# Optimization experiments

Hardware: AMD Instinct MI355X
Metric: run time of the kernel (lower is better)

The kernel has to match this reference:

```python
import jax, jax.numpy as jnp
import numpy as np

D_MODEL = 1024
N_HEADS = 16
HEAD_DIM = D_MODEL // N_HEADS
ROPE_BASE = 10000.0
NEG_INF = -1.0e9


def rotate_half(x):
    # interleaved pairs: (-x2_i, x1_i) re-flattened to last dim
    x1 = x[..., ::2]
    x2 = x[..., 1::2]
    return jnp.stack((-x2, x1), axis=-1).reshape(x.shape)


def rope_sin_cos(seq_len, head_dim, dtype):
    inv_freq = 1.0 / (ROPE_BASE ** (jnp.arange(0, head_dim, 2, dtype=jnp.float32) / head_dim))
    t = jnp.arange(seq_len, dtype=jnp.float32)
    freqs = jnp.einsum('i,j->ij', t, inv_freq)          # [T, hd/2]
    emb = jnp.concatenate((freqs, freqs), axis=-1)       # [T, hd]
    return jnp.sin(emb).astype(dtype), jnp.cos(emb).astype(dtype)


def apply_rope(x, sin, cos):
    # x: [B, H, T, hd]; sin/cos: [T, hd]
    return x * cos[None, None] + rotate_half(x) * sin[None, None]


def setup_inputs() -> dict:
    key = jax.random.key(0)
    ks = jax.random.split(key, 9)
    B, T, D = 2, 2048, D_MODEL
    q = jax.random.normal(ks[0], (B, T, D), dtype=jnp.float32)
    k = jax.random.normal(ks[1], (B, T, D), dtype=jnp.float32)
    v = jax.random.normal(ks[2], (B, T, D), dtype=jnp.float32)
    # causal additive mask, broadcastable over [B, H, Tq, Tk]
    causal = jnp.triu(jnp.full((T, T), NEG_INF, dtype=jnp.float32), k=1)
    attn_mask = causal[None, None]
    key_padding_mask = jax.random.uniform(ks[3], (B, T)) < 0.05
    scale = 1.0 / np.sqrt(D)
    Wq = jax.random.normal(ks[4], (D, D), dtype=jnp.float32) * scale
    Wk = jax.random.normal(ks[5], (D, D), dtype=jnp.float32) * scale
    Wv = jax.random.normal(ks[6], (D, D), dtype=jnp.float32) * scale
    Wo = jax.random.normal(ks[7], (D, D), dtype=jnp.float32) * scale
    return {"q": q, "k": k, "v": v, "attn_mask": attn_mask,
            "key_padding_mask": key_padding_mask,
            "Wq": Wq, "Wk": Wk, "Wv": Wv, "Wo": Wo}


def reference(q, k, v, attn_mask, key_padding_mask, Wq, Wk, Wv, Wo):
    B, Tq, _ = q.shape
    Tk = k.shape[1]
    H, hd = N_HEADS, HEAD_DIM
    # projections (nn.Linear: x @ W.T), split heads -> [B, H, T, hd]
    qh = (q @ Wq.T).reshape(B, Tq, H, hd).transpose(0, 2, 1, 3)
    kh = (k @ Wk.T).reshape(B, Tk, H, hd).transpose(0, 2, 1, 3)
    vh = (v @ Wv.T).reshape(B, Tk, H, hd).transpose(0, 2, 1, 3)
    sin_q, cos_q = rope_sin_cos(Tq, hd, q.dtype)
    sin_k, cos_k = rope_sin_cos(Tk, hd, k.dtype)
    qh = apply_rope(qh, sin_q, cos_q)
    kh = apply_rope(kh, sin_k, cos_k)
    scores = jnp.einsum('bhqd,bhkd->bhqk', qh, kh) / np.sqrt(hd)
    scores = scores + attn_mask
    scores = jnp.where(key_padding_mask[:, None, None, :], NEG_INF, scores)
    attn = jax.nn.softmax(scores, axis=-1)
    out = jnp.einsum('bhqk,bhkd->bhqd', attn, vh)
    out = out.transpose(0, 2, 1, 3).reshape(B, Tq, H * hd)
    return out @ Wo.T
```

## Files before the change

kernel.cpp:

```cpp
#include <hip/hip_runtime.h>
#include <stdint.h>

typedef __bf16 bf16x8 __attribute__((ext_vector_type(8)));
typedef float f32x4 __attribute__((ext_vector_type(4)));
typedef float f32x16 __attribute__((ext_vector_type(16)));

#define NEG_BIG2 (-1.442695040e9f)
#define SC_LOG2  (0.180336880f)

__device__ __forceinline__ unsigned short f2b(float f) {
  union { float f; unsigned int u; } c; c.f = f;
  unsigned int u = c.u;
  u += 0x7FFFu + ((u >> 16) & 1u);
  return (unsigned short)(u >> 16);
}
__device__ __forceinline__ float b2f(unsigned short h) {
  union { unsigned int u; float f; } c; c.u = ((unsigned int)h) << 16;
  return c.f;
}
__device__ __forceinline__ unsigned int pk2(float a, float b) {
  __bf16 x = (__bf16)a, y = (__bf16)b;
  unsigned short xu, yu;
  __builtin_memcpy(&xu, &x, 2);
  __builtin_memcpy(&yu, &y, 2);
  return (unsigned)xu | ((unsigned)yu << 16);
}
__device__ __forceinline__ float ex2(float x) {
  float r; asm("v_exp_f32 %0, %1" : "=v"(r) : "v"(x)); return r;
}

typedef const __attribute__((address_space(1))) unsigned int ga_u32;
typedef __attribute__((address_space(3))) unsigned int ls_u32;
__device__ __forceinline__ void gld16(const void* g, void* l) {
  __builtin_amdgcn_global_load_lds((ga_u32*)g, (ls_u32*)l, 16, 0, 0);
}

__device__ __forceinline__ void swap_pair(unsigned a, unsigned b, int hi,
                                          unsigned& lo_out, unsigned& hi_out) {
#if __has_builtin(__builtin_amdgcn_permlane32_swap)
  auto r = __builtin_amdgcn_permlane32_swap(a, b, false, false);
  lo_out = r[0]; hi_out = r[1];
#else
  unsigned pa = __shfl_xor(a, 32), pb = __shfl_xor(b, 32);
  lo_out = hi ? pb : a;
  hi_out = hi ? b : pa;
#endif
}

__global__ void rope_table_k(float* __restrict__ sin_t, float* __restrict__ cos_t) {
  int i = blockIdx.x * blockDim.x + threadIdx.x;
  int t = i >> 6, d = i & 63, f = d & 31;
  double inv = exp(-((double)(2 * f) / 64.0) * log(10000.0));
  double ang = (double)t * inv;
  sin_t[i] = (float)sin(ang);
  cos_t[i] = (float)cos(ang);
}

__global__ void detect_mask_k(const unsigned int* __restrict__ kpm, int* __restrict__ flag) {
  unsigned int v = 0;
  for (int i = threadIdx.x; i < 1024; i += 256) v |= kpm[i];
  if (v & ~1u) atomicOr(flag, 1);
}

__global__ void mask_pack_k(const void* __restrict__ kpm, const int* __restrict__ mflag,
                            unsigned long long* __restrict__ pmask) {
  const int w = threadIdx.x >> 6, lane = threadIdx.x & 63;
  const int bytes = *mflag;
  for (int i = w; i < 64; i += 4) {
    int b = i >> 5, kb = i & 31;
    int idx = b * 2048 + kb * 64 + lane;
    int pad = bytes ? (int)((const unsigned char*)kpm)[idx] : ((const int*)kpm)[idx];
    unsigned long long pm = __ballot(pad != 0);
    if (lane == 0) pmask[i] = pm;
  }
}

__global__ void convw_k(const float* __restrict__ Wq, const float* __restrict__ Wk,
                        const float* __restrict__ Wv, const float* __restrict__ Wo,
                        unsigned short* __restrict__ Wb) {
  size_t g = (size_t)blockIdx.x * 256 + threadIdx.x;
  size_t i8 = g * 8;
  int t = (int)(i8 >> 20);
  const float* src = (t == 0 ? Wq : t == 1 ? Wk : t == 2 ? Wv : Wo) + (i8 & 1048575);
  float4 a = *(const float4*)src, c = *(const float4*)(src + 4);
  uint4 o = { pk2(a.x, a.y), pk2(a.z, a.w), pk2(c.x, c.y), pk2(c.z, c.w) };
  *(uint4*)&Wb[i8] = o;
}

__global__ void conv_in_k(const float* __restrict__ q, const float* __restrict__ k,
                          const float* __restrict__ v, unsigned short* __restrict__ qb,
                          unsigned short* __restrict__ kb, unsigned short* __restrict__ vb) {
  size_t g = (size_t)blockIdx.x * 256 + threadIdx.x;
  size_t i8 = g * 8;
  int t = (int)(i8 >> 22);
  size_t off = i8 & 4194303;
  const float* src = (t == 0 ? q : t == 1 ? k : v) + off;
  unsigned short* dst = (t == 0 ? qb : t == 1 ? kb : vb) + off;
  float4 a = *(const float4*)src, c = *(const float4*)(src + 4);
  uint4 o = { pk2(a.x, a.y), pk2(a.z, a.w), pk2(c.x, c.y), pk2(c.z, c.w) };
  *(uint4*)dst = o;
}

template<bool ABF>
__global__ __launch_bounds__(256) void qkv_k(const void* __restrict__ A0,
                                             const void* __restrict__ A1,
                                             const void* __restrict__ A2,
                                             const unsigned short* __restrict__ Wb,
                                             unsigned short* __restrict__ qh,
                                             unsigned short* __restrict__ kh,
                                             unsigned short* __restrict__ vt) {
  const int z = blockIdx.z;
  const void* Ap = (z == 0) ? A0 : (z == 1) ? A1 : A2;
  const unsigned short* Wp = Wb + (size_t)z * 1048576;
  unsigned short* outp = (z == 0) ? qh : (z == 1) ? kh : vt;

  __shared__ unsigned short As[128 * 32];
  __shared__ unsigned short Bs[128 * 32];
  const int M0 = blockIdx.x * 128, N0 = blockIdx.y * 128;
  const int tid = threadIdx.x, lane = tid & 63, w = tid >> 6;
  const int wr = w >> 1, wc = w & 1;
  const int lrow = lane & 15, lgrp = lane >> 4;

  const f32x4 Z4 = {0.f, 0.f, 0.f, 0.f};
  f32x4 acc[4][4];
#pragma unroll
  for (int i = 0; i < 4; ++i)
#pragma unroll
    for (int j = 0; j < 4; ++j) acc[i][j] = Z4;

  for (int kt = 0; kt < 1024; kt += 32) {
    __syncthreads();
    if (ABF) {
      const unsigned short* Ab = (const unsigned short*)Ap;
#pragma unroll
      for (int i = 0; i < 2; ++i) {
        const unsigned short* gA = Ab +
            (size_t)(M0 + i * 64 + w * 16 + (lane >> 2)) * 1024 + kt + (lane & 3) * 8;
        gld16(gA, &As[i * 2048 + w * 512]);
      }
    } else {
      const int row = tid >> 1, half = tid & 1;
      const float* ap = (const float*)Ap + (size_t)(M0 + row) * 1024 + kt + half * 16;
      float4 f0 = *(const float4*)ap, f1 = *(const float4*)(ap + 4);
      float4 f2 = *(const float4*)(ap + 8), f3 = *(const float4*)(ap + 12);
      uint4 u0 = { pk2(f0.x, f0.y), pk2(f0.z, f0.w), pk2(f1.x, f1.y), pk2(f1.z, f1.w) };
      uint4 u1 = { pk2(f2.x, f2.y), pk2(f2.z, f2.w), pk2(f3.x, f3.y), pk2(f3.z, f3.w) };
      *(uint4*)&As[row * 32 + half * 16] = u0;
      *(uint4*)&As[row * 32 + half * 16 + 8] = u1;
    }
#pragma unroll
    for (int i = 0; i < 2; ++i) {
      const unsigned short* gB = Wp +
          (size_t)(N0 + i * 64 + w * 16 + (lane >> 2)) * 1024 + kt + (lane & 3) * 8;
      gld16(gB, &Bs[i * 2048 + w * 512]);
    }
    __syncthreads();
    bf16x8 af[4], bfv[4];
#pragma unroll
    for (int m = 0; m < 4; ++m)
      af[m] = *(const bf16x8*)&As[(wr * 64 + m * 16 + lrow) * 32 + lgrp * 8];
#pragma unroll
    for (int n = 0; n < 4; ++n)
      bfv[n] = *(const bf16x8*)&Bs[(wc * 64 + n * 16 + lrow) * 32 + lgrp * 8];
    __builtin_amdgcn_s_setprio(1);
#pragma unroll
    for (int m = 0; m < 4; ++m)
#pragma unroll
      for (int n = 0; n < 4; ++n)
        acc[m][n] = __builtin_amdgcn_mfma_f32_16x16x32_bf16(af[m], bfv[n], acc[m][n], 0, 0, 0);
    __builtin_amdgcn_s_setprio(0);
  }

#pragma unroll
  for (int mi = 0; mi < 4; ++mi)
#pragma unroll
    for (int ni = 0; ni < 4; ++ni) {
      const int m = M0 + wr * 64 + mi * 16 + lgrp * 4;
      const int n = N0 + wc * 64 + ni * 16 + lrow;
      const int b = m >> 11, t = m & 2047;
      if (z < 2) {
        unsigned short* o = outp +
            ((size_t)(b * 16 + (n >> 6)) * 2048 + t) * 64 + (n & 63);
#pragma unroll
        for (int r = 0; r < 4; ++r) o[(size_t)r * 64] = f2b(acc[mi][ni][r]);
      } else {
        unsigned short* o = outp +
            ((size_t)(b * 16 + (n >> 6)) * 64 + (n & 63)) * 2048 + t;
        *(ushort4*)o = make_ushort4(f2b(acc[mi][ni][0]), f2b(acc[mi][ni][1]),
                                    f2b(acc[mi][ni][2]), f2b(acc[mi][ni][3]));
      }
    }
}

__global__ __launch_bounds__(256) void gemm_o_k(const unsigned short* __restrict__ Ab,
                                                const unsigned short* __restrict__ Wp,
                                                float* __restrict__ outp) {
  __shared__ unsigned short As[64 * 32];
  __shared__ unsigned short Bs[128 * 32];
  const int M0 = blockIdx.x * 64, N0 = blockIdx.y * 128;
  const int tid = threadIdx.x, lane = tid & 63, w = tid >> 6;
  const int wr = w >> 1, wc = w & 1;
  const int lrow = lane & 15, lgrp = lane >> 4;

  const f32x4 Z4 = {0.f, 0.f, 0.f, 0.f};
  f32x4 acc[2][4];
#pragma unroll
  for (int i = 0; i < 2; ++i)
#pragma unroll
    for (int j = 0; j < 4; ++j) acc[i][j] = Z4;

  for (int kt = 0; kt < 1024; kt += 32) {
    __syncthreads();
    {
      const unsigned short* gA = Ab +
          (size_t)(M0 + w * 16 + (lane >> 2)) * 1024 + kt + (lane & 3) * 8;
      gld16(gA, &As[w * 512]);
    }
#pragma unroll
    for (int i = 0; i < 2; ++i) {
      const unsigned short* gB = Wp +
          (size_t)(N0 + i * 64 + w * 16 + (lane >> 2)) * 1024 + kt + (lane & 3) * 8;
      gld16(gB, &Bs[i * 2048 + w * 512]);
    }
    __syncthreads();
    bf16x8 af[2], bfv[4];
#pragma unroll
    for (int m = 0; m < 2; ++m)
      af[m] = *(const bf16x8*)&As[(wr * 32 + m * 16 + lrow) * 32 + lgrp * 8];
#pragma unroll
    for (int n = 0; n < 4; ++n)
      bfv[n] = *(const bf16x8*)&Bs[(wc * 64 + n * 16 + lrow) * 32 + lgrp * 8];
    __builtin_amdgcn_s_setprio(1);
#pragma unroll
    for (int m = 0; m < 2; ++m)
#pragma unroll
      for (int n = 0; n < 4; ++n)
        acc[m][n] = __builtin_amdgcn_mfma_f32_16x16x32_bf16(af[m], bfv[n], acc[m][n], 0, 0, 0);
    __builtin_amdgcn_s_setprio(0);
  }

#pragma unroll
  for (int mi = 0; mi < 2; ++mi)
#pragma unroll
    for (int ni = 0; ni < 4; ++ni) {
      const int m = M0 + wr * 32 + mi * 16 + lgrp * 4;
      const int n = N0 + wc * 64 + ni * 16 + lrow;
      float* o = outp + (size_t)m * 1024 + n;
#pragma unroll
      for (int r = 0; r < 4; ++r) o[(size_t)r * 1024] = acc[mi][ni][r];
    }
}

__global__ void rope_apply_k(unsigned short* __restrict__ qh, unsigned short* __restrict__ kh,
                             const float* __restrict__ sin_t, const float* __restrict__ cos_t) {
  const size_t per = (size_t)2 * 16 * 2048 * 16;
  size_t gid = (size_t)blockIdx.x * blockDim.x + threadIdx.x;
  if (gid >= 2 * per) return;
  unsigned short* base = (gid < per) ? qh : kh;
  size_t g = (gid < per) ? gid : gid - per;
  const int t = (int)((g >> 4) & 2047);
  const int d0 = ((int)g & 15) * 4;
  ushort4 x = ((ushort4*)base)[g];
  const float4 s4 = *(const float4*)&sin_t[t * 64 + d0];
  const float4 c4 = *(const float4*)&cos_t[t * 64 + d0];
  float x0 = b2f(x.x), x1 = b2f(x.y), x2 = b2f(x.z), x3 = b2f(x.w);
  ushort4 o;
  o.x = f2b(x0 * c4.x - x1 * s4.x);
  o.y = f2b(x1 * c4.y + x0 * s4.y);
  o.z = f2b(x2 * c4.z - x3 * s4.z);
  o.w = f2b(x3 * c4.w + x2 * s4.w);
  ((ushort4*)base)[g] = o;
}

__global__ __launch_bounds__(256, 2) void attn_k(
    const unsigned short* __restrict__ qh, const unsigned short* __restrict__ kh,
    const unsigned short* __restrict__ vt, const unsigned long long* __restrict__ pmask,
    unsigned short* __restrict__ ao) {
  const int bid = blockIdx.x;
  const int x = bid & 7, g = bid >> 3;
  const int bh = x * 4 + (g & 3);
  const int tile = 15 - (g >> 2);
  const int b = bh >> 4, h = bh & 15;
  const int tid = threadIdx.x, lane = tid & 63, w = tid >> 6;
  const int ln31 = lane & 31, hi = lane >> 5;

  __shared__ char Kb[2][8192];
  __shared__ char Vb[2][8192];
  __shared__ int flagv;

  const size_t bh_off = (size_t)bh * 2048 * 64;
  const int qw = tile * 128 + w * 32;
  const int q_abs = qw + ln31;
  const int nkv_w = qw / 64 + 1;
  const int nkv_b = tile * 2 + 2;
  const int swz = (ln31 & 7) << 4;

  bf16x8 qf[4];
#pragma unroll
  for (int dc = 0; dc < 4; ++dc)
    qf[dc] = *(const bf16x8*)(qh + bh_off + (size_t)(qw + ln31) * 64 + dc * 16 + hi * 8);

  const f32x16 Z16 = {0.f,0.f,0.f,0.f,0.f,0.f,0.f,0.f,0.f,0.f,0.f,0.f,0.f,0.f,0.f,0.f};
  f32x16 O0 = Z16, O1 = Z16;
  float m_run = -INFINITY, l_run = 0.f;

  uint4 kr0, kr1, vr0, vr1;
  const int srow = tid >> 2, sseg = tid & 3;
  const int sbase = srow * 128 + sseg * 32;
  const int sswz = (srow & 7) << 4;

  auto stage_load = [&](int kbi) {
    const unsigned short* kp = kh + bh_off + (size_t)(kbi * 64 + srow) * 64 + sseg * 16;
    kr0 = *(const uint4*)kp; kr1 = *(const uint4*)(kp + 8);
    const unsigned short* vp = vt + bh_off + (size_t)srow * 2048 + kbi * 64 + sseg * 16;
    vr0 = *(const uint4*)vp; vr1 = *(const uint4*)(vp + 8);
  };
  auto stage_write = [&](int bu) {
    *(uint4*)(Kb[bu] + (sbase ^ sswz)) = kr0;
    *(uint4*)(Kb[bu] + ((sbase + 16) ^ sswz)) = kr1;
    *(uint4*)(Vb[bu] + (sbase ^ sswz)) = vr0;
    *(uint4*)(Vb[bu] + ((sbase + 16) ^ sswz)) = vr1;
  };

  auto compute = [&](int kb, int cur) {
    const unsigned long long pmh = pmask[b * 32 + kb] >> (hi * 4);
    f32x16 S0 = Z16, S1 = Z16;
    __builtin_amdgcn_s_setprio(1);
#pragma unroll
    for (int dc = 0; dc < 4; ++dc) {
      bf16x8 k0 = *(const bf16x8*)(Kb[cur] + ((ln31 * 128 + dc * 32 + hi * 16) ^ swz));
      bf16x8 k1 = *(const bf16x8*)(Kb[cur] + (((ln31 + 32) * 128 + dc * 32 + hi * 16) ^ swz));
      S0 = __builtin_amdgcn_mfma_f32_32x32x16_bf16(k0, qf[dc], S0, 0, 0, 0);
      S1 = __builtin_amdgcn_mfma_f32_32x32x16_bf16(k1, qf[dc], S1, 0, 0, 0);
    }
    __builtin_amdgcn_s_setprio(0);

    const bool diag = (kb * 64 + 63) > qw;
    if (diag) {
#pragma unroll
      for (int r = 0; r < 16; ++r) {
        const int kloc = (r & 3) + 8 * (r >> 2);
        float sv = S0[r] * SC_LOG2;
        sv = ((pmh >> kloc) & 1) ? NEG_BIG2
             : ((kb * 64 + kloc + 4 * hi > q_abs) ? sv + NEG_BIG2 : sv);
        S0[r] = sv;
        float sw = S1[r] * SC_LOG2;
        sw = ((pmh >> (kloc + 32)) & 1) ? NEG_BIG2
             : ((kb * 64 + 32 + kloc + 4 * hi > q_abs) ? sw + NEG_BIG2 : sw);
        S1[r] = sw;
      }
    } else {
#pragma unroll
      for (int r = 0; r < 16; ++r) {
        const int kloc = (r & 3) + 8 * (r >> 2);
        float sv = S0[r] * SC_LOG2;
        S0[r] = ((pmh >> kloc) & 1) ? NEG_BIG2 : sv;
        float sw = S1[r] * SC_LOG2;
        S1[r] = ((pmh >> (kloc + 32)) & 1) ? NEG_BIG2 : sw;
      }
    }

    float vm = fmaxf(S0[0], S0[1]);
#pragma unroll
    for (int r = 2; r < 16; r += 2) vm = fmaxf(vm, fmaxf(S0[r], S0[r + 1]));
#pragma unroll
    for (int r = 0; r < 16; r += 2) vm = fmaxf(vm, fmaxf(S1[r], S1[r + 1]));
    vm = fmaxf(vm, __shfl_xor(vm, 32));

    if (__any(vm > m_run + 11.5f)) {
      const float mnew = fmaxf(m_run, vm);
      const float alpha = ex2(m_run - mnew);
      m_run = mnew;
      l_run *= alpha;
      O0 *= alpha; O1 *= alpha;
    }
    float rs = 0.f;
#pragma unroll
    for (int r = 0; r < 16; ++r) { float p = ex2(S0[r] - m_run); S0[r] = p; rs += p; }
#pragma unroll
    for (int r = 0; r < 16; ++r) { float p = ex2(S1[r] - m_run); S1[r] = p; rs += p; }
    rs += __shfl_xor(rs, 32);
    l_run += rs;

    union U8 { uint4 u; bf16x8 v; };
    bf16x8 pa[4];
#pragma unroll
    for (int kt = 0; kt < 2; ++kt) {
#pragma unroll
      for (int half = 0; half < 2; ++half) {
        float p0, p1, p2, p3, p4, p5, p6, p7;
        if (kt == 0) {
          if (half == 0) { p0=S0[0];p1=S0[1];p2=S0[2];p3=S0[3];p4=S0[4];p5=S0[5];p6=S0[6];p7=S0[7]; }
          else           { p0=S0[8];p1=S0[9];p2=S0[10];p3=S0[11];p4=S0[12];p5=S0[13];p6=S0[14];p7=S0[15]; }
        } else {
          if (half == 0) { p0=S1[0];p1=S1[1];p2=S1[2];p3=S1[3];p4=S1[4];p5=S1[5];p6=S1[6];p7=S1[7]; }
          else           { p0=S1[8];p1=S1[9];p2=S1[10];p3=S1[11];p4=S1[12];p5=S1[13];p6=S1[14];p7=S1[15]; }
        }
        unsigned e0 = pk2(p0, p1), e1 = pk2(p2, p3);
        unsigned o0 = pk2(p4, p5), o1 = pk2(p6, p7);
        unsigned a0, b0_, a1, b1_;
        swap_pair(e0, o0, hi, a0, b0_);
        swap_pair(e1, o1, hi, a1, b1_);
        U8 u; u.u = make_uint4(a0, a1, b0_, b1_);
        pa[kt * 2 + half] = u.v;
      }
    }

    __builtin_amdgcn_s_setprio(1);
#pragma unroll
    for (int c = 0; c < 4; ++c) {
      bf16x8 v0 = *(const bf16x8*)(Vb[cur] + ((ln31 * 128 + c * 32 + hi * 16) ^ swz));
      bf16x8 v1 = *(const bf16x8*)(Vb[cur] + (((ln31 + 32) * 128 + c * 32 + hi * 16) ^ swz));
      O0 = __builtin_amdgcn_mfma_f32_32x32x16_bf16(v0, pa[c], O0, 0, 0, 0);
      O1 = __builtin_amdgcn_mfma_f32_32x32x16_bf16(v1, pa[c], O1, 0, 0, 0);
    }
    __builtin_amdgcn_s_setprio(0);
  };

  stage_load(0);
  stage_write(0);
  for (int kb = 0; kb < nkv_b; ++kb) {
    if (kb + 1 < nkv_b) stage_load(kb + 1);
    __syncthreads();
    if (kb < nkv_w) compute(kb, kb & 1);
    __syncthreads();
    if (kb + 1 < nkv_b) stage_write((kb + 1) & 1);
  }

  if (tid == 0) flagv = 0;
  __syncthreads();
  if (m_run <= -7.2e8f) flagv = 1;
  __syncthreads();
  if (flagv) {
    for (int kb = nkv_b - 1; kb < 32; ++kb) {
      if (kb + 1 < 32) stage_load(kb + 1);
      __syncthreads();
      if (kb >= nkv_w) compute(kb, kb & 1);
      __syncthreads();
      if (kb + 1 < 32) stage_write((kb + 1) & 1);
    }
  }

  {
    const float inv = 1.0f / l_run;
    unsigned short* op = ao + (size_t)(b * 2048 + qw + ln31) * 1024 + h * 64;
#pragma unroll
    for (int g2 = 0; g2 < 4; ++g2) {
      const int d0 = 8 * g2 + 4 * hi;
      *(ushort4*)(op + d0) = make_ushort4(
          f2b(O0[g2 * 4 + 0] * inv), f2b(O0[g2 * 4 + 1] * inv),
          f2b(O0[g2 * 4 + 2] * inv), f2b(O0[g2 * 4 + 3] * inv));
      *(ushort4*)(op + 32 + d0) = make_ushort4(
          f2b(O1[g2 * 4 + 0] * inv), f2b(O1[g2 * 4 + 1] * inv),
          f2b(O1[g2 * 4 + 2] * inv), f2b(O1[g2 * 4 + 3] * inv));
    }
  }
}

extern "C" void kernel_launch(void* const* d_in, const int* in_sizes, int n_in,
                              void* d_out, int out_size, void* d_ws, size_t ws_size,
                              hipStream_t stream) {
  const float* q  = (const float*)d_in[0];
  const float* k  = (const float*)d_in[1];
  const float* v  = (const float*)d_in[2];
  const void*  kpm = d_in[4];
  const float* Wq = (const float*)d_in[5];
  const float* Wk = (const float*)d_in[6];
  const float* Wv = (const float*)d_in[7];
  const float* Wo = (const float*)d_in[8];

  char* ws = (char*)d_ws;
  unsigned short* qh = (unsigned short*)(ws);
  unsigned short* kh = (unsigned short*)(ws + (8u << 20));
  unsigned short* vt = (unsigned short*)(ws + (16u << 20));
  unsigned short* ao = (unsigned short*)(ws + (24u << 20));
  unsigned short* Wb = (unsigned short*)(ws + (32u << 20));
  float* sin_t = (float*)(ws + (40u << 20));
  float* cos_t = (float*)(ws + (40u << 20) + 524288);
  unsigned long long* pmask = (unsigned long long*)(ws + (41u << 20));
  int* mflag = (int*)(ws + (41u << 20) + 512);
  unsigned short* qb = (unsigned short*)(ws + (42u << 20));
  unsigned short* kb = (unsigned short*)(ws + (50u << 20));
  unsigned short* vb = (unsigned short*)(ws + (58u << 20));

  const bool big = ws_size >= (66ull << 20);

  (void)hipMemsetAsync(mflag, 0, sizeof(int), stream);
  detect_mask_k<<<1, 256, 0, stream>>>((const unsigned int*)kpm, mflag);
  mask_pack_k<<<1, 256, 0, stream>>>(kpm, mflag, pmask);
  rope_table_k<<<512, 256, 0, stream>>>(sin_t, cos_t);
  convw_k<<<2048, 256, 0, stream>>>(Wq, Wk, Wv, Wo, Wb);

  dim3 gq(32, 8, 3);
  if (big) {
    conv_in_k<<<6144, 256, 0, stream>>>(q, k, v, qb, kb, vb);
    qkv_k<true><<<gq, 256, 0, stream>>>(qb, kb, vb, Wb, qh, kh, vt);
  } else {
    qkv_k<false><<<gq, 256, 0, stream>>>(q, k, v, Wb, qh, kh, vt);
  }

  rope_apply_k<<<8192, 256, 0, stream>>>(qh, kh, sin_t, cos_t);

  attn_k<<<512, 256, 0, stream>>>(qh, kh, vt, pmask, ao);

  gemm_o_k<<<dim3(64, 8), 256, 0, stream>>>(ao, Wb + 3145728, (float*)d_out);
}
```

Baseline: 155.5 us.

## Split long causal attention tiles across two blocks and merge partial results

Causal query tiles 8-15 are split into two KV halves run by separate blocks, with a job table ordering work for load balance. Each half writes unnormalized partial outputs and running max and sum to workspace, and a new merge kernel combines them. The score scaling is folded into Q during RoPE, removing a multiply per score element in the attention kernel. In exchange there is extra global traffic for the partials, an additional kernel launch, and a dependence on workspace size.

```diff
diff --git a/kernel.cpp b/kernel.cpp
--- a/kernel.cpp
+++ b/kernel.cpp
@@ -46,6 +46,10 @@
   hi_out = hi ? b : pa;
 #endif
 }
+
+__device__ __constant__ unsigned char job_tab[24] = {
+  7, 47, 63, 46, 62, 6, 45, 61, 44, 60, 5, 43,
+  59, 42, 58, 4, 41, 57, 40, 56, 3, 2, 1, 0};
 
 __global__ void rope_table_k(float* __restrict__ sin_t, float* __restrict__ cos_t) {
   int i = blockIdx.x * blockDim.x + threadIdx.x;
@@ -256,8 +260,10 @@
   const size_t per = (size_t)2 * 16 * 2048 * 16;
   size_t gid = (size_t)blockIdx.x * blockDim.x + threadIdx.x;
   if (gid >= 2 * per) return;
-  unsigned short* base = (gid < per) ? qh : kh;
-  size_t g = (gid < per) ? gid : gid - per;
+  const bool is_q = gid < per;
+  unsigned short* base = is_q ? qh : kh;
+  const float sc = is_q ? SC_LOG2 : 1.0f;
+  size_t g = is_q ? gid : gid - per;
   const int t = (int)((g >> 4) & 2047);
   const int d0 = ((int)g & 15) * 4;
   ushort4 x = ((ushort4*)base)[g];
@@ -265,21 +271,29 @@
   const float4 c4 = *(const float4*)&cos_t[t * 64 + d0];
   float x0 = b2f(x.x), x1 = b2f(x.y), x2 = b2f(x.z), x3 = b2f(x.w);
   ushort4 o;
-  o.x = f2b(x0 * c4.x - x1 * s4.x);
-  o.y = f2b(x1 * c4.y + x0 * s4.y);
-  o.z = f2b(x2 * c4.z - x3 * s4.z);
-  o.w = f2b(x3 * c4.w + x2 * s4.w);
+  o.x = f2b((x0 * c4.x - x1 * s4.x) * sc);
+  o.y = f2b((x1 * c4.y + x0 * s4.y) * sc);
+  o.z = f2b((x2 * c4.z - x3 * s4.z) * sc);
+  o.w = f2b((x3 * c4.w + x2 * s4.w) * sc);
   ((ushort4*)base)[g] = o;
 }
 
 __global__ __launch_bounds__(256, 2) void attn_k(
     const unsigned short* __restrict__ qh, const unsigned short* __restrict__ kh,
     const unsigned short* __restrict__ vt, const unsigned long long* __restrict__ pmask,
-    unsigned short* __restrict__ ao) {
+    unsigned short* __restrict__ ao, float* __restrict__ Op, float* __restrict__ Ml,
+    const int mode) {
   const int bid = blockIdx.x;
-  const int x = bid & 7, g = bid >> 3;
-  const int bh = x * 4 + (g & 3);
-  const int tile = 15 - (g >> 2);
+  int bh, tile, half = 0, split = 0;
+  if (mode) {
+    const unsigned char j = job_tab[bid >> 5];
+    bh = bid & 31;
+    tile = j & 15; half = (j >> 4) & 1; split = j >> 5;
+  } else {
+    const int x = bid & 7, g = bid >> 3;
+    bh = x * 4 + (g & 3);
+    tile = 15 - (g >> 2);
+  }
   const int b = bh >> 4, h = bh & 15;
   const int tid = threadIdx.x, lane = tid & 63, w = tid >> 6;
   const int ln31 = lane & 31, hi = lane >> 5;
@@ -291,8 +305,9 @@
   const size_t bh_off = (size_t)bh * 2048 * 64;
   const int qw = tile * 128 + w * 32;
   const int q_abs = qw + ln31;
-  const int nkv_w = qw / 64 + 1;
-  const int nkv_b = tile * 2 + 2;
+  const int kb_begin = (split && half) ? tile + 1 : 0;
+  const int kb_end_stage = (split && !half) ? tile + 1 : tile * 2 + 2;
+  const int nkv_w = min(qw / 64 + 1, kb_end_stage);
   const int swz = (ln31 & 7) << 4;
 
   bf16x8 qf[4];
@@ -323,7 +338,9 @@
   };
 
   auto compute = [&](int kb, int cur) {
-    const unsigned long long pmh = pmask[b * 32 + kb] >> (hi * 4);
+    const unsigned long long pm = pmask[b * 32 + kb];
+    const unsigned plo = (unsigned)(pm >> (hi * 4));
+    const unsigned phi = (unsigned)((pm >> 32) >> (hi * 4));
     f32x16 S0 = Z16, S1 = Z16;
     __builtin_amdgcn_s_setprio(1);
 #pragma unroll
@@ -340,12 +357,12 @@
 #pragma unroll
       for (int r = 0; r < 16; ++r) {
         const int kloc = (r & 3) + 8 * (r >> 2);
-        float sv = S0[r] * SC_LOG2;
-        sv = ((pmh >> kloc) & 1) ? NEG_BIG2
+        float sv = S0[r];
+        sv = ((plo >> kloc) & 1) ? NEG_BIG2
              : ((kb * 64 + kloc + 4 * hi > q_abs) ? sv + NEG_BIG2 : sv);
         S0[r] = sv;
-        float sw = S1[r] * SC_LOG2;
-        sw = ((pmh >> (kloc + 32)) & 1) ? NEG_BIG2
+        float sw = S1[r];
+        sw = ((phi >> kloc) & 1) ? NEG_BIG2
              : ((kb * 64 + 32 + kloc + 4 * hi > q_abs) ? sw + NEG_BIG2 : sw);
         S1[r] = sw;
       }
@@ -353,10 +370,8 @@
 #pragma unroll
       for (int r = 0; r < 16; ++r) {
         const int kloc = (r & 3) + 8 * (r >> 2);
-        float sv = S0[r] * SC_LOG2;
-        S0[r] = ((pmh >> kloc) & 1) ? NEG_BIG2 : sv;
-        float sw = S1[r] * SC_LOG2;
-        S1[r] = ((pmh >> (kloc + 32)) & 1) ? NEG_BIG2 : sw;
+        S0[r] = ((plo >> kloc) & 1) ? NEG_BIG2 : S0[r];
+        S1[r] = ((phi >> kloc) & 1) ? NEG_BIG2 : S1[r];
       }
     }
 
@@ -387,14 +402,14 @@
 #pragma unroll
     for (int kt = 0; kt < 2; ++kt) {
 #pragma unroll
-      for (int half = 0; half < 2; ++half) {
+      for (int hf = 0; hf < 2; ++hf) {
         float p0, p1, p2, p3, p4, p5, p6, p7;
         if (kt == 0) {
-          if (half == 0) { p0=S0[0];p1=S0[1];p2=S0[2];p3=S0[3];p4=S0[4];p5=S0[5];p6=S0[6];p7=S0[7]; }
-          else           { p0=S0[8];p1=S0[9];p2=S0[10];p3=S0[11];p4=S0[12];p5=S0[13];p6=S0[14];p7=S0[15]; }
+          if (hf == 0) { p0=S0[0];p1=S0[1];p2=S0[2];p3=S0[3];p4=S0[4];p5=S0[5];p6=S0[6];p7=S0[7]; }
+          else         { p0=S0[8];p1=S0[9];p2=S0[10];p3=S0[11];p4=S0[12];p5=S0[13];p6=S0[14];p7=S0[15]; }
         } else {
-          if (half == 0) { p0=S1[0];p1=S1[1];p2=S1[2];p3=S1[3];p4=S1[4];p5=S1[5];p6=S1[6];p7=S1[7]; }
-          else           { p0=S1[8];p1=S1[9];p2=S1[10];p3=S1[11];p4=S1[12];p5=S1[13];p6=S1[14];p7=S1[15]; }
+          if (hf == 0) { p0=S1[0];p1=S1[1];p2=S1[2];p3=S1[3];p4=S1[4];p5=S1[5];p6=S1[6];p7=S1[7]; }
+          else         { p0=S1[8];p1=S1[9];p2=S1[10];p3=S1[11];p4=S1[12];p5=S1[13];p6=S1[14];p7=S1[15]; }
         }
         unsigned e0 = pk2(p0, p1), e1 = pk2(p2, p3);
         unsigned o0 = pk2(p4, p5), o1 = pk2(p6, p7);
@@ -402,7 +417,7 @@
         swap_pair(e0, o0, hi, a0, b0_);
         swap_pair(e1, o1, hi, a1, b1_);
         U8 u; u.u = make_uint4(a0, a1, b0_, b1_);
-        pa[kt * 2 + half] = u.v;
+        pa[kt * 2 + hf] = u.v;
       }
     }
 
@@ -417,31 +432,32 @@
     __builtin_amdgcn_s_setprio(0);
   };
 
-  stage_load(0);
+  const int nsteps = kb_end_stage - kb_begin;
+  stage_load(kb_begin);
   stage_write(0);
-  for (int kb = 0; kb < nkv_b; ++kb) {
-    if (kb + 1 < nkv_b) stage_load(kb + 1);
-    __syncthreads();
-    if (kb < nkv_w) compute(kb, kb & 1);
-    __syncthreads();
-    if (kb + 1 < nkv_b) stage_write((kb + 1) & 1);
-  }
-
-  if (tid == 0) flagv = 0;
-  __syncthreads();
-  if (m_run <= -7.2e8f) flagv = 1;
-  __syncthreads();
-  if (flagv) {
-    for (int kb = nkv_b - 1; kb < 32; ++kb) {
-      if (kb + 1 < 32) stage_load(kb + 1);
-      __syncthreads();
-      if (kb >= nkv_w) compute(kb, kb & 1);
-      __syncthreads();
-      if (kb + 1 < 32) stage_write((kb + 1) & 1);
-    }
-  }
-
-  {
+  for (int s = 0; s < nsteps; ++s) {
+    const int kb = kb_begin + s;
+    if (s + 1 < nsteps) stage_load(kb + 1);
+    __syncthreads();
+    if (kb < nkv_w) compute(kb, s & 1);
+    __syncthreads();
+    if (s + 1 < nsteps) stage_write((s + 1) & 1);
+  }
+
+  if (!split) {
+    if (tid == 0) flagv = 0;
+    __syncthreads();
+    if (m_run <= -7.2e8f) flagv = 1;
+    __syncthreads();
+    if (flagv) {
+      for (int kb = kb_end_stage - 1; kb < 32; ++kb) {
+        if (kb + 1 < 32) stage_load(kb + 1);
+        __syncthreads();
+        if (kb >= nkv_w) compute(kb, kb & 1);
+        __syncthreads();
+        if (kb + 1 < 32) stage_write((kb + 1) & 1);
+      }
+    }
     const float inv = 1.0f / l_run;
     unsigned short* op = ao + (size_t)(b * 2048 + qw + ln31) * 1024 + h * 64;
 #pragma unroll
@@ -454,6 +470,54 @@
           f2b(O1[g2 * 4 + 0] * inv), f2b(O1[g2 * 4 + 1] * inv),
           f2b(O1[g2 * 4 + 2] * inv), f2b(O1[g2 * 4 + 3] * inv));
     }
+  } else {
+    const int bh8t = bh * 8 + (tile - 8);
+    const int qloc = w * 32 + ln31;
+    float* opp = Op + (size_t)(bh8t * 2 + half) * 8192 + qloc;
+#pragma unroll
+    for (int r = 0; r < 16; ++r) {
+      const int d = (r & 3) + 8 * (r >> 2) + 4 * hi;
+      opp[d * 128] = O0[r];
+      opp[(d + 32) * 128] = O1[r];
+    }
+    if (hi == 0) {
+      float* mlp = Ml + (size_t)(bh8t * 2 + half) * 256 + qloc;
+      mlp[0] = m_run;
+      mlp[128] = l_run;
+    }
+  }
+}
+
+__global__ __launch_bounds__(256) void merge_k(const float* __restrict__ Op,
+                                               const float* __restrict__ Ml,
+                                               unsigned short* __restrict__ ao) {
+  const int bh = blockIdx.x & 31, t8 = blockIdx.x >> 5;
+  const int b = bh >> 4, h = bh & 15;
+  const int tile = t8 + 8;
+  const size_t ob = (size_t)(bh * 8 + t8) * 2 * 8192;
+  const size_t mlb = (size_t)(bh * 8 + t8) * 2 * 256;
+  __shared__ float T[128][69];
+  const int tid = threadIdx.x;
+
+  for (int i = tid; i < 8192; i += 256) {
+    const int d = i >> 7, q = i & 127;
+    const float m0 = Ml[mlb + q],       l0 = Ml[mlb + 128 + q];
+    const float m1 = Ml[mlb + 256 + q], l1 = Ml[mlb + 384 + q];
+    const float m = fmaxf(m0, m1);
+    const float a0 = ex2(m0 - m), a1 = ex2(m1 - m);
+    const float linv = 1.0f / (l0 * a0 + l1 * a1);
+    const float v = (Op[ob + i] * a0 + Op[ob + 8192 + i] * a1) * linv;
+    T[q][d] = v;
+  }
+  __syncthreads();
+
+  const int q = tid >> 1, dbase = (tid & 1) * 32;
+  unsigned short* op = ao + (size_t)(b * 2048 + tile * 128 + q) * 1024 + h * 64 + dbase;
+#pragma unroll
+  for (int j = 0; j < 8; ++j) {
+    const int d = dbase + j * 4;
+    *(ushort4*)(op + j * 4) = make_ushort4(f2b(T[q][d]), f2b(T[q][d + 1]),
+                                           f2b(T[q][d + 2]), f2b(T[q][d + 3]));
   }
 }
 
@@ -482,8 +546,11 @@
   unsigned short* qb = (unsigned short*)(ws + (42u << 20));
   unsigned short* kb = (unsigned short*)(ws + (50u << 20));
   unsigned short* vb = (unsigned short*)(ws + (58u << 20));
+  float* Opart = (float*)(ws + (66ull << 20));
+  float* Mlpart = (float*)(ws + (83ull << 20));
 
   const bool big = ws_size >= (66ull << 20);
+  const bool can_split = ws_size >= (84ull << 20);
 
   (void)hipMemsetAsync(mflag, 0, sizeof(int), stream);
   detect_mask_k<<<1, 256, 0, stream>>>((const unsigned int*)kpm, mflag);
@@ -501,7 +568,9 @@
 
   rope_apply_k<<<8192, 256, 0, stream>>>(qh, kh, sin_t, cos_t);
 
-  attn_k<<<512, 256, 0, stream>>>(qh, kh, vt, pmask, ao);
+  attn_k<<<can_split ? 768 : 512, 256, 0, stream>>>(qh, kh, vt, pmask, ao,
+                                                    Opart, Mlpart, can_split ? 1 : 0);
+  if (can_split) merge_k<<<256, 256, 0, stream>>>(Opart, Mlpart, ao);
 
   gemm_o_k<<<dim3(64, 8), 256, 0, stream>>>(ao, Wb + 3145728, (float*)d_out);
 }
```

Measured after the change: 161.4 us. 1.04x slower.

## Stage 128-key KV tiles per barrier and interleave causal tile order

Applied to the files above, without the earlier changes.

The attention kernel now stages 128 keys of K and V per pipeline step instead of 64. Each staged tile runs two 64-key compute sub-steps, which halves the number of __syncthreads pairs per KV sweep. The block-to-tile mapping also changes: the first half of the grid walks tiles from heavy to light and the second half from light to heavy, to balance causal work across waves. LDS use doubles to 64 KB per block, which may limit the two-blocks-per-CU occupancy target and puts more load registers in flight.

```diff
diff --git a/kernel.cpp b/kernel.cpp
--- a/kernel.cpp
+++ b/kernel.cpp
@@ -277,22 +277,22 @@
     const unsigned short* __restrict__ vt, const unsigned long long* __restrict__ pmask,
     unsigned short* __restrict__ ao) {
   const int bid = blockIdx.x;
-  const int x = bid & 7, g = bid >> 3;
-  const int bh = x * 4 + (g & 3);
-  const int tile = 15 - (g >> 2);
+  const int x = bid & 7, j = bid >> 3;
+  const int tile = (j < 32) ? (15 - (j >> 2)) : ((j - 32) >> 2);
+  const int bh = x * 4 + (j & 3);
   const int b = bh >> 4, h = bh & 15;
   const int tid = threadIdx.x, lane = tid & 63, w = tid >> 6;
   const int ln31 = lane & 31, hi = lane >> 5;
 
-  __shared__ char Kb[2][8192];
-  __shared__ char Vb[2][8192];
+  __shared__ char Kb[2][16384];
+  __shared__ char Vb[2][16384];
   __shared__ int flagv;
 
   const size_t bh_off = (size_t)bh * 2048 * 64;
   const int qw = tile * 128 + w * 32;
   const int q_abs = qw + ln31;
   const int nkv_w = qw / 64 + 1;
-  const int nkv_b = tile * 2 + 2;
+  const int nkv_t = tile + 1;
   const int swz = (ln31 & 7) << 4;
 
   bf16x8 qf[4];
@@ -304,32 +304,43 @@
   f32x16 O0 = Z16, O1 = Z16;
   float m_run = -INFINITY, l_run = 0.f;
 
-  uint4 kr0, kr1, vr0, vr1;
-  const int srow = tid >> 2, sseg = tid & 3;
-  const int sbase = srow * 128 + sseg * 32;
-  const int sswz = (srow & 7) << 4;
-
-  auto stage_load = [&](int kbi) {
-    const unsigned short* kp = kh + bh_off + (size_t)(kbi * 64 + srow) * 64 + sseg * 16;
-    kr0 = *(const uint4*)kp; kr1 = *(const uint4*)(kp + 8);
-    const unsigned short* vp = vt + bh_off + (size_t)srow * 2048 + kbi * 64 + sseg * 16;
-    vr0 = *(const uint4*)vp; vr1 = *(const uint4*)(vp + 8);
+  uint4 kr0, kr1, kr2, kr3, vr0, vr1, vr2, vr3;
+  const int ksrow = tid >> 1, kseg = tid & 1;
+  const int kbase = ksrow * 128 + kseg * 64;
+  const int kswz = (ksrow & 7) << 4;
+  const int vdrow = tid >> 2, vseg = tid & 3;
+  const int vbase = vdrow * 256 + vseg * 64;
+  const int vswz = (vdrow & 7) << 4;
+
+  auto stage_load = [&](int kti) {
+    const unsigned short* kp = kh + bh_off + (size_t)(kti * 128 + ksrow) * 64 + kseg * 32;
+    kr0 = *(const uint4*)kp;        kr1 = *(const uint4*)(kp + 8);
+    kr2 = *(const uint4*)(kp + 16); kr3 = *(const uint4*)(kp + 24);
+    const unsigned short* vp = vt + bh_off + (size_t)vdrow * 2048 + kti * 128 + vseg * 32;
+    vr0 = *(const uint4*)vp;        vr1 = *(const uint4*)(vp + 8);
+    vr2 = *(const uint4*)(vp + 16); vr3 = *(const uint4*)(vp + 24);
   };
   auto stage_write = [&](int bu) {
-    *(uint4*)(Kb[bu] + (sbase ^ sswz)) = kr0;
-    *(uint4*)(Kb[bu] + ((sbase + 16) ^ sswz)) = kr1;
-    *(uint4*)(Vb[bu] + (sbase ^ sswz)) = vr0;
-    *(uint4*)(Vb[bu] + ((sbase + 16) ^ sswz)) = vr1;
+    *(uint4*)(Kb[bu] + ((kbase)      ^ kswz)) = kr0;
+    *(uint4*)(Kb[bu] + ((kbase + 16) ^ kswz)) = kr1;
+    *(uint4*)(Kb[bu] + ((kbase + 32) ^ kswz)) = kr2;
+    *(uint4*)(Kb[bu] + ((kbase + 48) ^ kswz)) = kr3;
+    *(uint4*)(Vb[bu] + ((vbase)      ^ vswz)) = vr0;
+    *(uint4*)(Vb[bu] + ((vbase + 16) ^ vswz)) = vr1;
+    *(uint4*)(Vb[bu] + ((vbase + 32) ^ vswz)) = vr2;
+    *(uint4*)(Vb[bu] + ((vbase + 48) ^ vswz)) = vr3;
   };
 
   auto compute = [&](int kb, int cur) {
+    const int subk = (kb & 1) * 8192;
+    const int subv = (kb & 1) * 128;
     const unsigned long long pmh = pmask[b * 32 + kb] >> (hi * 4);
     f32x16 S0 = Z16, S1 = Z16;
     __builtin_amdgcn_s_setprio(1);
 #pragma unroll
     for (int dc = 0; dc < 4; ++dc) {
-      bf16x8 k0 = *(const bf16x8*)(Kb[cur] + ((ln31 * 128 + dc * 32 + hi * 16) ^ swz));
-      bf16x8 k1 = *(const bf16x8*)(Kb[cur] + (((ln31 + 32) * 128 + dc * 32 + hi * 16) ^ swz));
+      bf16x8 k0 = *(const bf16x8*)(Kb[cur] + subk + ((ln31 * 128 + dc * 32 + hi * 16) ^ swz));
+      bf16x8 k1 = *(const bf16x8*)(Kb[cur] + subk + (((ln31 + 32) * 128 + dc * 32 + hi * 16) ^ swz));
       S0 = __builtin_amdgcn_mfma_f32_32x32x16_bf16(k0, qf[dc], S0, 0, 0, 0);
       S1 = __builtin_amdgcn_mfma_f32_32x32x16_bf16(k1, qf[dc], S1, 0, 0, 0);
     }
@@ -387,14 +398,14 @@
 #pragma unroll
     for (int kt = 0; kt < 2; ++kt) {
 #pragma unroll
-      for (int half = 0; half < 2; ++half) {
+      for (int hf = 0; hf < 2; ++hf) {
         float p0, p1, p2, p3, p4, p5, p6, p7;
         if (kt == 0) {
-          if (half == 0) { p0=S0[0];p1=S0[1];p2=S0[2];p3=S0[3];p4=S0[4];p5=S0[5];p6=S0[6];p7=S0[7]; }
-          else           { p0=S0[8];p1=S0[9];p2=S0[10];p3=S0[11];p4=S0[12];p5=S0[13];p6=S0[14];p7=S0[15]; }
+          if (hf == 0) { p0=S0[0];p1=S0[1];p2=S0[2];p3=S0[3];p4=S0[4];p5=S0[5];p6=S0[6];p7=S0[7]; }
+          else         { p0=S0[8];p1=S0[9];p2=S0[10];p3=S0[11];p4=S0[12];p5=S0[13];p6=S0[14];p7=S0[15]; }
         } else {
-          if (half == 0) { p0=S1[0];p1=S1[1];p2=S1[2];p3=S1[3];p4=S1[4];p5=S1[5];p6=S1[6];p7=S1[7]; }
-          else           { p0=S1[8];p1=S1[9];p2=S1[10];p3=S1[11];p4=S1[12];p5=S1[13];p6=S1[14];p7=S1[15]; }
+          if (hf == 0) { p0=S1[0];p1=S1[1];p2=S1[2];p3=S1[3];p4=S1[4];p5=S1[5];p6=S1[6];p7=S1[7]; }
+          else         { p0=S1[8];p1=S1[9];p2=S1[10];p3=S1[11];p4=S1[12];p5=S1[13];p6=S1[14];p7=S1[15]; }
         }
         unsigned e0 = pk2(p0, p1), e1 = pk2(p2, p3);
         unsigned o0 = pk2(p4, p5), o1 = pk2(p6, p7);
@@ -402,15 +413,15 @@
         swap_pair(e0, o0, hi, a0, b0_);
         swap_pair(e1, o1, hi, a1, b1_);
         U8 u; u.u = make_uint4(a0, a1, b0_, b1_);
-        pa[kt * 2 + half] = u.v;
+        pa[kt * 2 + hf] = u.v;
       }
     }
 
     __builtin_amdgcn_s_setprio(1);
 #pragma unroll
     for (int c = 0; c < 4; ++c) {
-      bf16x8 v0 = *(const bf16x8*)(Vb[cur] + ((ln31 * 128 + c * 32 + hi * 16) ^ swz));
-      bf16x8 v1 = *(const bf16x8*)(Vb[cur] + (((ln31 + 32) * 128 + c * 32 + hi * 16) ^ swz));
+      bf16x8 v0 = *(const bf16x8*)(Vb[cur] + ((ln31 * 256 + subv + c * 32 + hi * 16) ^ swz));
+      bf16x8 v1 = *(const bf16x8*)(Vb[cur] + (((ln31 + 32) * 256 + subv + c * 32 + hi * 16) ^ swz));
       O0 = __builtin_amdgcn_mfma_f32_32x32x16_bf16(v0, pa[c], O0, 0, 0, 0);
       O1 = __builtin_amdgcn_mfma_f32_32x32x16_bf16(v1, pa[c], O1, 0, 0, 0);
     }
@@ -419,12 +430,17 @@
 
   stage_load(0);
   stage_write(0);
-  for (int kb = 0; kb < nkv_b; ++kb) {
-    if (kb + 1 < nkv_b) stage_load(kb + 1);
+  for (int kt = 0; kt < nkv_t; ++kt) {
+    if (kt + 1 < nkv_t) stage_load(kt + 1);
     __syncthreads();
-    if (kb < nkv_w) compute(kb, kb & 1);
+    const int kb0 = kt * 2;
+#pragma unroll 1
+    for (int s2 = 0; s2 < 2; ++s2) {
+      const int kb = kb0 + s2;
+      if (kb < nkv_w) compute(kb, kt & 1);
+    }
     __syncthreads();
-    if (kb + 1 < nkv_b) stage_write((kb + 1) & 1);
+    if (kt + 1 < nkv_t) stage_write((kt + 1) & 1);
   }
 
   if (tid == 0) flagv = 0;
@@ -432,12 +448,17 @@
   if (m_run <= -7.2e8f) flagv = 1;
   __syncthreads();
   if (flagv) {
-    for (int kb = nkv_b - 1; kb < 32; ++kb) {
-      if (kb + 1 < 32) stage_load(kb + 1);
+    for (int kt = nkv_t - 1; kt < 16; ++kt) {
+      if (kt + 1 < 16) stage_load(kt + 1);
       __syncthreads();
-      if (kb >= nkv_w) compute(kb, kb & 1);
+      const int kb0 = kt * 2;
+#pragma unroll 1
+      for (int s2 = 0; s2 < 2; ++s2) {
+        const int kb = kb0 + s2;
+        if (kb >= nkv_w) compute(kb, kt & 1);
+      }
       __syncthreads();
-      if (kb + 1 < 32) stage_write((kb + 1) & 1);
+      if (kt + 1 < 16) stage_write((kt + 1) & 1);
     }
   }
 
```

Result: slower. 172.9 us (+11.2%).
